# Kernel tuning notes

Hardware: AMD Instinct MI355X
Metric: run time of the kernel (lower is better)

## Reference

```python
import math
import jax, jax.numpy as jnp
import numpy as np

N_HEADS = 16
D_EMBED = 1024
D_HEAD = D_EMBED // N_HEADS
B, S = 4, 2048


def setup_inputs() -> dict:
    key = jax.random.key(0)
    k1, k2, k3, k4, k5 = jax.random.split(key, 5)
    scale_in = 1.0 / math.sqrt(D_EMBED)
    return {
        "x": jax.random.normal(k1, (B, S, D_EMBED), dtype=jnp.float32),
        "w_in": jax.random.normal(k2, (3 * D_EMBED, D_EMBED), dtype=jnp.float32) * scale_in,
        "b_in": jax.random.normal(k3, (3 * D_EMBED,), dtype=jnp.float32) * 0.02,
        "w_out": jax.random.normal(k4, (D_EMBED, D_EMBED), dtype=jnp.float32) * scale_in,
        "b_out": jax.random.normal(k5, (D_EMBED,), dtype=jnp.float32) * 0.02,
        "causal_mask": 1,
    }


def reference(x, w_in, b_in, w_out, b_out, causal_mask):
    Bn, Sn, D = x.shape
    # fused QKV projection (torch Linear: x @ W.T + b)
    qkv = x @ w_in.T + b_in                       # (B, S, 3D)
    q, k, v = jnp.split(qkv, 3, axis=-1)
    def to_heads(t):
        return t.reshape(Bn, Sn, N_HEADS, D_HEAD).transpose(0, 2, 1, 3)  # (B,H,S,dh)
    q, k, v = to_heads(q), to_heads(k), to_heads(v)
    # manual scaled dot-product attention, full (B,H,S,S) scores
    scores = jnp.einsum("bhqd,bhkd->bhqk", q, k)
    if causal_mask:
        tri = jnp.triu(jnp.ones((Sn, Sn), dtype=bool), k=1)
        scores = jnp.where(tri, -jnp.inf, scores)
    scores = scores / math.sqrt(D_HEAD)
    weights = jax.nn.softmax(scores, axis=-1)
    out = jnp.einsum("bhqk,bhkd->bhqd", weights, v)  # (B,H,S,dh)
    out = out.transpose(0, 2, 1, 3).reshape(Bn, Sn, D)
    return out @ w_out.T + b_out
```

## Files before the change

### kernel.cpp

```cpp
#include <hip/hip_runtime.h>

typedef __bf16 bf16x8 __attribute__((ext_vector_type(8)));
typedef float  f32x4  __attribute__((ext_vector_type(4)));
typedef unsigned int uint;

__device__ inline unsigned short f2bf(float f) {
  union { float f; unsigned int u; } v; v.f = f;
  unsigned int u = v.u;
  unsigned int r = u + 0x7FFF + ((u >> 16) & 1);
  return (unsigned short)(r >> 16);
}

__device__ inline uint pack_bf16_rhu(float a, float b) {
  uint ua = __builtin_bit_cast(uint, a) + 0x8000u;
  uint ub = __builtin_bit_cast(uint, b) + 0x8000u;
  return __builtin_amdgcn_perm(ub, ua, 0x07060302u);
}

__device__ inline void load_lds16(const unsigned short* g, unsigned short* l) {
  __builtin_amdgcn_global_load_lds(
      (const __attribute__((address_space(1))) uint*)(g),
      (__attribute__((address_space(3))) uint*)(l), 16, 0, 0);
}

__device__ inline void cvt4(const float* in, unsigned short* out) {
  float4 f = *reinterpret_cast<const float4*>(in);
  ushort4 o;
  o.x = f2bf(f.x); o.y = f2bf(f.y); o.z = f2bf(f.z); o.w = f2bf(f.w);
  *reinterpret_cast<ushort4*>(out) = o;
}

__global__ void cvt_all(const float* __restrict__ x, const float* __restrict__ w_in,
                        const float* __restrict__ w_out,
                        unsigned short* __restrict__ x_bf,
                        unsigned short* __restrict__ w_in_bf,
                        unsigned short* __restrict__ w_out_bf) {
  const int n1 = 8192 * 1024, n2 = 3072 * 1024;
  int i = (blockIdx.x * blockDim.x + threadIdx.x) * 4;
  if (i < n1)            cvt4(x + i, x_bf + i);
  else if (i < n1 + n2)  cvt4(w_in + (i - n1), w_in_bf + (i - n1));
  else                   cvt4(w_out + (i - n1 - n2), w_out_bf + (i - n1 - n2));
}

template<bool OUT_BF16, bool VSPLIT>
__global__ __launch_bounds__(256) void gemm_bt128(
    const unsigned short* __restrict__ A,
    const unsigned short* __restrict__ B,
    const float* __restrict__ bias,
    void* __restrict__ Cout,
    unsigned short* __restrict__ vt,
    int M, int N, int K, int ldc, float scale, int ncut)
{
  __shared__ __attribute__((aligned(16))) unsigned short As[128 * 64];
  __shared__ __attribute__((aligned(16))) unsigned short Bs[128 * 64];

  const int t    = threadIdx.x;
  const int wave = t >> 6, lane = t & 63;
  const int l16  = lane & 15, quad = lane >> 4;
  const int wr = wave >> 1, wc = wave & 1;
  const int m0 = blockIdx.y * 128, n0 = blockIdx.x * 128;
  const int l8 = l16 & 7;

  f32x4 acc[4][4] = {};

  for (int k0 = 0; k0 < K; k0 += 64) {
#pragma unroll
    for (int i = 0; i < 4; ++i) {
      int chunk = i * 256 + t;
      int row = chunk >> 3, cb = chunk & 7;
      int gcb = cb ^ (row & 7);
      load_lds16(A + (size_t)(m0 + row) * K + k0 + gcb * 8, As + chunk * 8);
    }
#pragma unroll
    for (int i = 0; i < 4; ++i) {
      int chunk = i * 256 + t;
      int row = chunk >> 3, cb = chunk & 7;
      int gcb = cb ^ (row & 7);
      load_lds16(B + (size_t)(n0 + row) * K + k0 + gcb * 8, Bs + chunk * 8);
    }
    __syncthreads();
#pragma unroll
    for (int ks = 0; ks < 2; ++ks) {
      bf16x8 af[4], bfr[4];
#pragma unroll
      for (int mt = 0; mt < 4; ++mt)
        af[mt] = *(const bf16x8*)(As + (wr * 64 + mt * 16 + l16) * 64 +
                                  (((ks * 4 + quad) ^ l8) << 3));
#pragma unroll
      for (int nt = 0; nt < 4; ++nt)
        bfr[nt] = *(const bf16x8*)(Bs + (wc * 64 + nt * 16 + l16) * 64 +
                                   (((ks * 4 + quad) ^ l8) << 3));
#pragma unroll
      for (int mt = 0; mt < 4; ++mt)
#pragma unroll
        for (int nt = 0; nt < 4; ++nt)
          acc[mt][nt] = __builtin_amdgcn_mfma_f32_16x16x32_bf16(af[mt], bfr[nt], acc[mt][nt], 0, 0, 0);
    }
    __syncthreads();
  }

#pragma unroll
  for (int nt = 0; nt < 4; ++nt) {
    int col = n0 + wc * 64 + nt * 16 + l16;
    float bv = bias[col];
    float mlt = (col < ncut) ? scale : 1.0f;
#pragma unroll
    for (int mt = 0; mt < 4; ++mt) {
      int row0 = m0 + wr * 64 + mt * 16 + quad * 4;
      float v0 = (acc[mt][nt][0] + bv) * mlt;
      float v1 = (acc[mt][nt][1] + bv) * mlt;
      float v2 = (acc[mt][nt][2] + bv) * mlt;
      float v3 = (acc[mt][nt][3] + bv) * mlt;
      if (VSPLIT && col >= 2048) {
        int d = col - 2048, h = d >> 6, dd = d & 63;
        int bb = row0 >> 11, s = row0 & 2047;
        uint2 w;
        w.x = pack_bf16_rhu(v0, v1);
        w.y = pack_bf16_rhu(v2, v3);
        *(uint2*)(vt + ((size_t)((bb * 16 + h) * 64 + dd) * 2048 + s)) = w;
      } else {
#pragma unroll
        for (int r = 0; r < 4; ++r) {
          float v = (r == 0) ? v0 : (r == 1) ? v1 : (r == 2) ? v2 : v3;
          if (OUT_BF16)
            ((unsigned short*)Cout)[(size_t)(row0 + r) * ldc + col] = f2bf(v);
          else
            ((float*)Cout)[(size_t)(row0 + r) * ldc + col] = v;
        }
      }
    }
  }
}

__global__ __launch_bounds__(256) void attn(
    const unsigned short* __restrict__ qkv2,
    const unsigned short* __restrict__ vt,
    unsigned short* __restrict__ y,
    const int* __restrict__ flag)
{
  __shared__ __attribute__((aligned(16))) unsigned short Qs[64 * 64];
  __shared__ __attribute__((aligned(16))) unsigned short Ks[64 * 64];
  __shared__ __attribute__((aligned(16))) unsigned short VtF[64 * 64];

  const int t    = threadIdx.x;
  const int wave = t >> 6, lane = t & 63;
  const int l16  = lane & 15, quad = lane >> 4;
  const int l8   = l16 & 7;
  const int idx = blockIdx.x;
  const int bh  = idx & 63;
  const int qt  = 31 - (idx >> 6);
  const int b = bh >> 4, h = bh & 15;
  const int causal = flag[0];
  const int q0 = qt * 64;

  const unsigned short* Qg = qkv2 + (size_t)b * 2048 * 2048 + h * 64;
  const unsigned short* Kg = Qg + 1024;
  const unsigned short* Vtg = vt + (size_t)bh * 64 * 2048;

  const int sr = t >> 2, sg = (t & 3) * 2;
  const int slot0 = sr * 64 + (((sg    ) ^ (sr & 7)) << 3);
  const int slot1 = sr * 64 + (((sg + 1) ^ (sr & 7)) << 3);
  const int vb = t & 3;
  const int vslot0 = sr * 64 + ((( vb     ) ^ (sr & 7)) << 3);
  const int vslot1 = sr * 64 + (((vb + 4) ^ (sr & 7)) << 3);
  const unsigned short* vrow = Vtg + (size_t)sr * 2048;

  {
    const unsigned short* src = Qg + (size_t)(q0 + sr) * 2048 + sg * 8;
    *(uint4*)(Qs + slot0) = *(const uint4*)src;
    *(uint4*)(Qs + slot1) = *(const uint4*)(src + 8);
  }
  __syncthreads();
  bf16x8 qf[2];
  qf[0] = *(const bf16x8*)(Qs + (wave * 16 + l16) * 64 + (((0 * 4 + quad) ^ l8) << 3));
  qf[1] = *(const bf16x8*)(Qs + (wave * 16 + l16) * 64 + (((1 * 4 + quad) ^ l8) << 3));
  __syncthreads();
  unsigned short* Ps = Qs;

  f32x4 ot[4] = {};
  float l_lane = 0.f;
  const int q_glob = q0 + wave * 16 + l16;
  const int jmax = causal ? qt : 31;

  uint4 kreg0, kreg1, vreg0, vreg1;
  {
    const unsigned short* src = Kg + (size_t)sr * 2048 + sg * 8;
    kreg0 = *(const uint4*)src;
    kreg1 = *(const uint4*)(src + 8);
    vreg0 = *(const uint4*)(vrow + vb * 8);
    vreg1 = *(const uint4*)(vrow + vb * 8 + 32);
  }

  for (int j = 0; j <= jmax; ++j) {
    *(uint4*)(Ks + slot0)   = kreg0;
    *(uint4*)(Ks + slot1)   = kreg1;
    *(uint4*)(VtF + vslot0) = vreg0;
    *(uint4*)(VtF + vslot1) = vreg1;
    __syncthreads();

    if (j < jmax) {
      const int kvn = (j + 1) * 64;
      const unsigned short* src = Kg + (size_t)(kvn + sr) * 2048 + sg * 8;
      kreg0 = *(const uint4*)src;
      kreg1 = *(const uint4*)(src + 8);
      vreg0 = *(const uint4*)(vrow + kvn + vb * 8);
      vreg1 = *(const uint4*)(vrow + kvn + vb * 8 + 32);
    }

    f32x4 st[4] = {};
#pragma unroll
    for (int ks = 0; ks < 2; ++ks) {
#pragma unroll
      for (int mt = 0; mt < 4; ++mt) {
        bf16x8 kf = *(const bf16x8*)(Ks + (mt * 16 + l16) * 64 + (((ks * 4 + quad) ^ l8) << 3));
        st[mt] = __builtin_amdgcn_mfma_f32_16x16x32_bf16(kf, qf[ks], st[mt], 0, 0, 0);
      }
    }

    const bool diag = (causal != 0) && (j == qt);
    const int kv0 = j * 64;
#pragma unroll
    for (int mt = 0; mt < 4; ++mt) {
      float p[4];
#pragma unroll
      for (int r = 0; r < 4; ++r) {
        float pv = __builtin_amdgcn_exp2f(st[mt][r]);
        if (diag) {
          int kv = kv0 + mt * 16 + quad * 4 + r;
          if (kv > q_glob) pv = 0.f;
        }
        p[r] = pv;
      }
      l_lane += (p[0] + p[1]) + (p[2] + p[3]);
      uint2 w;
      w.x = pack_bf16_rhu(p[0], p[1]);
      w.y = pack_bf16_rhu(p[2], p[3]);
      *(uint2*)(Ps + (wave * 16 + l16) * 64 +
                ((((mt * 2 + (quad >> 1)) ^ l8) << 3) + (quad & 1) * 4)) = w;
    }
    __threadfence_block();

#pragma unroll
    for (int ks = 0; ks < 2; ++ks) {
      bf16x8 pf = *(const bf16x8*)(Ps + (wave * 16 + l16) * 64 + (((ks * 4 + quad) ^ l8) << 3));
#pragma unroll
      for (int mt = 0; mt < 4; ++mt) {
        bf16x8 vf = *(const bf16x8*)(VtF + (mt * 16 + l16) * 64 + (((ks * 4 + quad) ^ l8) << 3));
        ot[mt] = __builtin_amdgcn_mfma_f32_16x16x32_bf16(vf, pf, ot[mt], 0, 0, 0);
      }
    }
    __syncthreads();
  }

  l_lane += __shfl_xor(l_lane, 16);
  l_lane += __shfl_xor(l_lane, 32);
  float inv = 1.f / l_lane;

#pragma unroll
  for (int mt = 0; mt < 4; ++mt) {
    uint2 w;
    w.x = pack_bf16_rhu(ot[mt][0] * inv, ot[mt][1] * inv);
    w.y = pack_bf16_rhu(ot[mt][2] * inv, ot[mt][3] * inv);
    *(uint2*)(Ps + (wave * 16 + l16) * 64 +
              ((((mt * 2 + (quad >> 1)) ^ l8) << 3) + (quad & 1) * 4)) = w;
  }
  __syncthreads();
  {
    size_t base = ((size_t)b * 2048 + q0 + sr) * 1024 + h * 64 + sg * 8;
    *(uint4*)(y + base)     = *(const uint4*)(Ps + slot0);
    *(uint4*)(y + base + 8) = *(const uint4*)(Ps + slot1);
  }
}

extern "C" void kernel_launch(void* const* d_in, const int* in_sizes, int n_in,
                              void* d_out, int out_size, void* d_ws, size_t ws_size,
                              hipStream_t stream) {
  const float* x     = (const float*)d_in[0];
  const float* w_in  = (const float*)d_in[1];
  const float* b_in  = (const float*)d_in[2];
  const float* w_out = (const float*)d_in[3];
  const float* b_out = (const float*)d_in[4];
  const int*   cmask = (const int*)d_in[5];

  char* ws = (char*)d_ws;
  unsigned short* x_bf     = (unsigned short*)(ws);
  unsigned short* w_in_bf  = (unsigned short*)(ws + 16777216);
  unsigned short* w_out_bf = (unsigned short*)(ws + 23068672);
  unsigned short* qkv2_bf  = (unsigned short*)(ws + 25165824);
  unsigned short* vt_bf    = (unsigned short*)(ws + 58720256);
  unsigned short* y_bf     = (unsigned short*)(ws + 75497472);

  const int ntot = (8192 + 3072 + 1024) * 1024;
  cvt_all<<<dim3(ntot / 4 / 256), 256, 0, stream>>>(x, w_in, w_out, x_bf, w_in_bf, w_out_bf);

  gemm_bt128<true, true><<<dim3(24, 64), 256, 0, stream>>>(
      x_bf, w_in_bf, b_in, qkv2_bf, vt_bf, 8192, 3072, 1024, 2048,
      0.18033688011112042f, 1024);

  attn<<<dim3(2048), 256, 0, stream>>>(qkv2_bf, vt_bf, y_bf, cmask);

  gemm_bt128<false, false><<<dim3(8, 64), 256, 0, stream>>>(
      y_bf, w_out_bf, b_out, d_out, nullptr, 8192, 1024, 1024, 1024, 1.0f, 0);
}
```

Before: 246.7 us.

## Switch attention kernel to 32x32x16 MFMA with 2x2 wave tiling

Each of the four waves now owns a 32-query by 32-key (or head-dim) quadrant and uses 32x32x16 bf16 MFMAs instead of 16x16x32 ones. Q fragments are loaded straight from global memory into registers, which removes the LDS staging and its two barriers. Because P is now shared across waves, the per-wave threadfence becomes a full __syncthreads. The row sums are combined across the two key-half waves through a small LDS buffer at the end. The aim is fewer MFMA issues and fewer LDS fragment reads per tile, at the cost of an extra block barrier in every iteration.

```diff
diff --git a/kernel.cpp b/kernel.cpp
--- a/kernel.cpp
+++ b/kernel.cpp
@@ -2,6 +2,7 @@
 
 typedef __bf16 bf16x8 __attribute__((ext_vector_type(8)));
 typedef float  f32x4  __attribute__((ext_vector_type(4)));
+typedef float  f32x16 __attribute__((ext_vector_type(16)));
 typedef unsigned int uint;
 
 __device__ inline unsigned short f2bf(float f) {
@@ -138,48 +139,49 @@
     unsigned short* __restrict__ y,
     const int* __restrict__ flag)
 {
-  __shared__ __attribute__((aligned(16))) unsigned short Qs[64 * 64];
+  __shared__ __attribute__((aligned(16))) unsigned short P2[64 * 64];
   __shared__ __attribute__((aligned(16))) unsigned short Ks[64 * 64];
   __shared__ __attribute__((aligned(16))) unsigned short VtF[64 * 64];
+  __shared__ float Lbuf[2][2][32];
 
   const int t    = threadIdx.x;
   const int wave = t >> 6, lane = t & 63;
-  const int l16  = lane & 15, quad = lane >> 4;
-  const int l8   = l16 & 7;
+  const int l32  = lane & 31, hi = lane >> 5;
+  const int qh = wave & 1, kh = wave >> 1;
   const int idx = blockIdx.x;
   const int bh  = idx & 63;
   const int qt  = 31 - (idx >> 6);
   const int b = bh >> 4, h = bh & 15;
   const int causal = flag[0];
   const int q0 = qt * 64;
-
-  const unsigned short* Qg = qkv2 + (size_t)b * 2048 * 2048 + h * 64;
-  const unsigned short* Kg = Qg + 1024;
+  const int swz = l32 & 7;
+
+  const unsigned short* Qg  = qkv2 + (size_t)b * 2048 * 2048 + h * 64;
+  const unsigned short* Kg  = Qg + 1024;
   const unsigned short* Vtg = vt + (size_t)bh * 64 * 2048;
 
+  const int qrow_lds = qh * 32 + l32;
+  const int q_glob   = q0 + qrow_lds;
+
+  bf16x8 qf[4];
+  {
+    const unsigned short* qr = Qg + (size_t)q_glob * 2048 + hi * 8;
+    qf[0] = *(const bf16x8*)(qr);
+    qf[1] = *(const bf16x8*)(qr + 16);
+    qf[2] = *(const bf16x8*)(qr + 32);
+    qf[3] = *(const bf16x8*)(qr + 48);
+  }
+
   const int sr = t >> 2, sg = (t & 3) * 2;
-  const int slot0 = sr * 64 + (((sg    ) ^ (sr & 7)) << 3);
+  const int slot0 = sr * 64 + ((sg ^ (sr & 7)) << 3);
   const int slot1 = sr * 64 + (((sg + 1) ^ (sr & 7)) << 3);
   const int vb = t & 3;
-  const int vslot0 = sr * 64 + ((( vb     ) ^ (sr & 7)) << 3);
+  const int vslot0 = sr * 64 + ((vb ^ (sr & 7)) << 3);
   const int vslot1 = sr * 64 + (((vb + 4) ^ (sr & 7)) << 3);
   const unsigned short* vrow = Vtg + (size_t)sr * 2048;
 
-  {
-    const unsigned short* src = Qg + (size_t)(q0 + sr) * 2048 + sg * 8;
-    *(uint4*)(Qs + slot0) = *(const uint4*)src;
-    *(uint4*)(Qs + slot1) = *(const uint4*)(src + 8);
-  }
-  __syncthreads();
-  bf16x8 qf[2];
-  qf[0] = *(const bf16x8*)(Qs + (wave * 16 + l16) * 64 + (((0 * 4 + quad) ^ l8) << 3));
-  qf[1] = *(const bf16x8*)(Qs + (wave * 16 + l16) * 64 + (((1 * 4 + quad) ^ l8) << 3));
-  __syncthreads();
-  unsigned short* Ps = Qs;
-
-  f32x4 ot[4] = {};
+  f32x16 ot = {};
   float l_lane = 0.f;
-  const int q_glob = q0 + wave * 16 + l16;
   const int jmax = causal ? qt : 31;
 
   uint4 kreg0, kreg1, vreg0, vreg1;
@@ -207,26 +209,26 @@
       vreg1 = *(const uint4*)(vrow + kvn + vb * 8 + 32);
     }
 
-    f32x4 st[4] = {};
-#pragma unroll
-    for (int ks = 0; ks < 2; ++ks) {
-#pragma unroll
-      for (int mt = 0; mt < 4; ++mt) {
-        bf16x8 kf = *(const bf16x8*)(Ks + (mt * 16 + l16) * 64 + (((ks * 4 + quad) ^ l8) << 3));
-        st[mt] = __builtin_amdgcn_mfma_f32_16x16x32_bf16(kf, qf[ks], st[mt], 0, 0, 0);
+    f32x16 st = {};
+    {
+      const unsigned short* kbase = Ks + (kh * 32 + l32) * 64;
+#pragma unroll
+      for (int dstep = 0; dstep < 4; ++dstep) {
+        bf16x8 kf = *(const bf16x8*)(kbase + (((dstep * 2 + hi) ^ swz) << 3));
+        st = __builtin_amdgcn_mfma_f32_32x32x16_bf16(kf, qf[dstep], st, 0, 0, 0);
       }
     }
 
     const bool diag = (causal != 0) && (j == qt);
     const int kv0 = j * 64;
 #pragma unroll
-    for (int mt = 0; mt < 4; ++mt) {
+    for (int rr = 0; rr < 4; ++rr) {
       float p[4];
 #pragma unroll
       for (int r = 0; r < 4; ++r) {
-        float pv = __builtin_amdgcn_exp2f(st[mt][r]);
+        float pv = __builtin_amdgcn_exp2f(st[rr * 4 + r]);
         if (diag) {
-          int kv = kv0 + mt * 16 + quad * 4 + r;
+          int kv = kv0 + kh * 32 + rr * 8 + hi * 4 + r;
           if (kv > q_glob) pv = 0.f;
         }
         p[r] = pv;
@@ -235,40 +237,43 @@
       uint2 w;
       w.x = pack_bf16_rhu(p[0], p[1]);
       w.y = pack_bf16_rhu(p[2], p[3]);
-      *(uint2*)(Ps + (wave * 16 + l16) * 64 +
-                ((((mt * 2 + (quad >> 1)) ^ l8) << 3) + (quad & 1) * 4)) = w;
-    }
-    __threadfence_block();
-
-#pragma unroll
-    for (int ks = 0; ks < 2; ++ks) {
-      bf16x8 pf = *(const bf16x8*)(Ps + (wave * 16 + l16) * 64 + (((ks * 4 + quad) ^ l8) << 3));
-#pragma unroll
-      for (int mt = 0; mt < 4; ++mt) {
-        bf16x8 vf = *(const bf16x8*)(VtF + (mt * 16 + l16) * 64 + (((ks * 4 + quad) ^ l8) << 3));
-        ot[mt] = __builtin_amdgcn_mfma_f32_16x16x32_bf16(vf, pf, ot[mt], 0, 0, 0);
+      int G = kh * 4 + rr;
+      *(uint2*)(P2 + qrow_lds * 64 + (((G ^ swz) << 3) + hi * 4)) = w;
+    }
+    __syncthreads();
+
+    {
+      const unsigned short* vbase = VtF + (kh * 32 + l32) * 64;
+      const unsigned short* pbase = P2 + qrow_lds * 64;
+#pragma unroll
+      for (int kstep = 0; kstep < 4; ++kstep) {
+        int G = kstep * 2 + hi;
+        bf16x8 vf = *(const bf16x8*)(vbase + (((G ^ swz) << 3)));
+        bf16x8 pf = *(const bf16x8*)(pbase + (((G ^ swz) << 3)));
+        ot = __builtin_amdgcn_mfma_f32_32x32x16_bf16(vf, pf, ot, 0, 0, 0);
       }
     }
     __syncthreads();
   }
 
-  l_lane += __shfl_xor(l_lane, 16);
   l_lane += __shfl_xor(l_lane, 32);
-  float inv = 1.f / l_lane;
-
-#pragma unroll
-  for (int mt = 0; mt < 4; ++mt) {
+  Lbuf[qh][kh][l32] = l_lane;
+  __syncthreads();
+  const float inv = 1.f / (Lbuf[qh][0][l32] + Lbuf[qh][1][l32]);
+
+#pragma unroll
+  for (int rr = 0; rr < 4; ++rr) {
     uint2 w;
-    w.x = pack_bf16_rhu(ot[mt][0] * inv, ot[mt][1] * inv);
-    w.y = pack_bf16_rhu(ot[mt][2] * inv, ot[mt][3] * inv);
-    *(uint2*)(Ps + (wave * 16 + l16) * 64 +
-              ((((mt * 2 + (quad >> 1)) ^ l8) << 3) + (quad & 1) * 4)) = w;
+    w.x = pack_bf16_rhu(ot[rr * 4 + 0] * inv, ot[rr * 4 + 1] * inv);
+    w.y = pack_bf16_rhu(ot[rr * 4 + 2] * inv, ot[rr * 4 + 3] * inv);
+    int G = kh * 4 + rr;
+    *(uint2*)(P2 + qrow_lds * 64 + (((G ^ swz) << 3) + hi * 4)) = w;
   }
   __syncthreads();
   {
     size_t base = ((size_t)b * 2048 + q0 + sr) * 1024 + h * 64 + sg * 8;
-    *(uint4*)(y + base)     = *(const uint4*)(Ps + slot0);
-    *(uint4*)(y + base + 8) = *(const uint4*)(Ps + slot1);
+    *(uint4*)(y + base)     = *(const uint4*)(P2 + slot0);
+    *(uint4*)(y + base + 8) = *(const uint4*)(P2 + slot1);
   }
 }
 
```

Result: slower. 259.9 us (+5.4%).
